# Kernel tuning notes

Measured on AMD Instinct MI355X. Metric: run time of the kernel, lower is better.

Reference implementation:

```python
import jax, jax.numpy as jnp
import numpy as np

N, T, F_IN = 20000, 13, 3
E = 320000
NB, NL = 4, 2
C_RES, C_DIL, C_SKIP, C_END = 32, 32, 256, 512
KSZ, KHOP = 2, 4
N_PRED, N_OUT = 12, 2
L = NB * NL
DILS = [2 ** i for _ in range(NB) for i in range(NL)]  # [1,2,1,2,1,2,1,2]
EPS = 1e-5


def _dconv(x, w, d):
    # x: [N,C,T], w: [O,I,K]; valid dilated conv -> [N,O,T-(K-1)*d]
    return jax.lax.conv_general_dilated(x, w, (1,), 'VALID', rhs_dilation=(d,),
                                        dimension_numbers=('NCH', 'OIH', 'NCH'))


def _forward(inputs, edge_src, edge_dst, enter_w, enter_b, filt_w, filt_b, gate_w, gate_b,
             gc_w, gc_b, skip_w, skip_b, bn_g, bn_b, out1_w, out1_b, out2_w, out2_b):
    # inputs: [N,T,F] -> x: [N,C_RES,T] via 1x1 conv (enter)
    x = jnp.einsum('of,ntf->not', enter_w, inputs) + enter_b[None, :, None]
    deg = jax.ops.segment_sum(jnp.ones((E,), x.dtype), edge_dst, num_segments=N)
    deg = jnp.maximum(deg, 1.0)[:, None, None]

    def propagate(h):  # [N,t,C]: mean over incoming edges (normalized diffusion step)
        return jax.ops.segment_sum(h[edge_src], edge_dst, num_segments=N) / deg

    skip = jnp.zeros((N, C_SKIP, T), x.dtype)
    for l in range(L):
        d = DILS[l]
        f = jnp.tanh(_dconv(x, filt_w[l], d) + filt_b[l][None, :, None])
        g = jax.nn.sigmoid(_dconv(x, gate_w[l], d) + gate_b[l][None, :, None])
        h = f * g                                   # [N,C_DIL,t]
        t = h.shape[-1]
        skip = skip[..., -t:] + jnp.einsum('oc,nct->not', skip_w[l], h) + skip_b[l][None, :, None]
        # K-hop graph diffusion conv on [N,t,C]
        hh = h.transpose(0, 2, 1)
        acc = jnp.einsum('ntc,co->nto', hh, gc_w[l, 0])
        cur = hh
        for k in range(1, KHOP):
            cur = propagate(cur)
            acc = acc + jnp.einsum('ntc,co->nto', cur, gc_w[l, k])
        acc = acc + gc_b[l]
        x = acc.transpose(0, 2, 1) + x[..., -t:]    # residual add
        # BatchNorm1d over (N, t) per channel (training-mode batch stats)
        mu = x.mean(axis=(0, 2), keepdims=True)
        var = x.var(axis=(0, 2), keepdims=True)
        x = bn_g[l][None, :, None] * (x - mu) * jax.lax.rsqrt(var + EPS) + bn_b[l][None, :, None]
    y = jax.nn.relu(skip)                           # [N,C_SKIP,1]
    y = jax.nn.relu(jnp.einsum('oc,nct->not', out1_w, y) + out1_b[None, :, None])
    y = jnp.einsum('oc,nct->not', out2_w, y) + out2_b[None, :, None]  # [N,n_pred*n_out,1]
    return y.reshape(N, N_PRED, -1)


def setup_inputs() -> dict:
    key = jax.random.key(0)
    ks = jax.random.split(key, 12)
    s = 0.05
    f32 = jnp.float32
    return {
        'inputs': jax.random.normal(ks[0], (N, T, F_IN), f32),
        'edge_src': jax.random.randint(ks[1], (E,), 0, N),
        'edge_dst': jax.random.randint(ks[2], (E,), 0, N),
        'enter_w': jax.random.normal(ks[3], (C_RES, F_IN), f32) * s,
        'enter_b': jnp.zeros((C_RES,), f32),
        'filt_w': jax.random.normal(ks[4], (L, C_DIL, C_RES, KSZ), f32) * s,
        'filt_b': jnp.zeros((L, C_DIL), f32),
        'gate_w': jax.random.normal(ks[5], (L, C_DIL, C_RES, KSZ), f32) * s,
        'gate_b': jnp.zeros((L, C_DIL), f32),
        'gc_w': jax.random.normal(ks[6], (L, KHOP, C_DIL, C_RES), f32) * s,
        'gc_b': jnp.zeros((L, C_RES), f32),
        'skip_w': jax.random.normal(ks[7], (L, C_SKIP, C_DIL), f32) * s,
        'skip_b': jnp.zeros((L, C_SKIP), f32),
        'bn_g': jnp.ones((L, C_RES), f32),
        'bn_b': jnp.zeros((L, C_RES), f32),
        'out1_w': jax.random.normal(ks[8], (C_END, C_SKIP), f32) * s,
        'out1_b': jnp.zeros((C_END,), f32),
        'out2_w': jax.random.normal(ks[9], (N_PRED * N_OUT, C_END), f32) * s,
        'out2_b': jnp.zeros((N_PRED * N_OUT,), f32),
    }


def reference(inputs, edge_src, edge_dst, enter_w, enter_b, filt_w, filt_b, gate_w, gate_b,
              gc_w, gc_b, skip_w, skip_b, bn_g, bn_b, out1_w, out1_b, out2_w, out2_b):
    return _forward(inputs, edge_src, edge_dst, enter_w, enter_b, filt_w, filt_b, gate_w, gate_b,
                    gc_w, gc_b, skip_w, skip_b, bn_g, bn_b, out1_w, out1_b, out2_w, out2_b)
```

## Files before the change

### kernel.cpp

```cpp
#include <hip/hip_runtime.h>
#include <cmath>

constexpr int N = 20000, T = 13, E = 320000;
constexpr int NB_SCAN = (N + 255) / 256;
constexpr int NPART = 64;
typedef unsigned int uint32;

typedef __attribute__((ext_vector_type(8))) short short8;
typedef __attribute__((ext_vector_type(4))) float f32x4;

__device__ __forceinline__ unsigned short f2bf(float f) {
  unsigned int u = __float_as_uint(f);
  unsigned int r = (u + 0x7FFFu + ((u >> 16) & 1u)) >> 16;
  return (unsigned short)r;
}
__device__ __forceinline__ float bflo(uint32 v) { return __uint_as_float(v << 16); }
__device__ __forceinline__ float bfhi(uint32 v) { return __uint_as_float(v & 0xFFFF0000u); }
__device__ __forceinline__ uint32 packbf(float lo, float hi) {
  return (uint32)f2bf(lo) | ((uint32)f2bf(hi) << 16);
}

constexpr size_t WALIGN = 512;
constexpr size_t align_up(size_t x) { return (x + WALIGN - 1) & ~(WALIGN - 1); }

constexpr size_t XA_OFF  = 0;
constexpr size_t X_SZ    = align_up((size_t)N * 13 * 32 * 4);
constexpr size_t XB_OFF  = XA_OFF + X_SZ;
constexpr size_t H_OFF   = XB_OFF + X_SZ;
constexpr size_t H_SZ    = align_up((size_t)N * 12 * 32 * 4);
constexpr size_t C1_OFF  = H_OFF + H_SZ;
constexpr size_t C2_OFF  = C1_OFF + H_SZ;
constexpr size_t C3_OFF  = C2_OFF + H_SZ;
constexpr size_t HL_OFF  = C3_OFF + H_SZ;
constexpr size_t HL_SZ   = align_up((size_t)N * 256 * 4);
constexpr size_t WS2_OFF = HL_OFF + HL_SZ;
constexpr size_t SB_OFF  = WS2_OFF + align_up(256 * 256 * 4);
constexpr size_t SUMS_OFF = SB_OFF + align_up(256 * 4);
constexpr size_t PAR_OFF  = SUMS_OFF + align_up(8 * NPART * 64 * 4);
constexpr size_t CNT_OFF  = PAR_OFF + align_up(9 * 64 * 4);
constexpr size_t ROW_OFF  = CNT_OFF + align_up((size_t)N * 4);
constexpr size_t FILL_OFF = ROW_OFF + align_up((size_t)(N + 1) * 4);
constexpr size_t COL_OFF  = FILL_OFF + align_up((size_t)N * 4);
constexpr size_t DEG_OFF  = COL_OFF + align_up((size_t)E * 4);
constexpr size_t BP_OFF   = DEG_OFF + align_up((size_t)N * 4);
constexpr size_t CP_OFF   = BP_OFF + align_up(8 * 2048 * 4);
constexpr size_t BW1_OFF  = CP_OFF + align_up(8 * 2176 * 4);
constexpr size_t BW2_OFF  = BW1_OFF + align_up(32768 * 4);
constexpr size_t BS_OFF   = BW2_OFF + align_up(65536 * 4);
constexpr size_t BO_OFF   = BS_OFF + align_up((size_t)NB_SCAN * 4);
constexpr size_t S_OFF  = C2_OFF;

__global__ void k_count(const int* __restrict__ dst, int* __restrict__ cnt) {
  int i = blockIdx.x * 256 + threadIdx.x;
  if (i < E) atomicAdd(&cnt[dst[i]], 1);
}

__global__ __launch_bounds__(256) void k_scan1(const int* __restrict__ cnt, int* __restrict__ bsum) {
  __shared__ int sc[256];
  int t = threadIdx.x; int idx = blockIdx.x * 256 + t;
  int v = (idx < N) ? cnt[idx] : 0;
  sc[t] = v; __syncthreads();
  for (int off = 1; off < 256; off <<= 1) {
    int u = (t >= off) ? sc[t - off] : 0;
    __syncthreads();
    sc[t] += u;
    __syncthreads();
  }
  if (t == 255) bsum[blockIdx.x] = sc[255];
}

__global__ __launch_bounds__(256) void k_scan2(const int* __restrict__ bsum, int* __restrict__ boff) {
  __shared__ int sc[256];
  int t = threadIdx.x;
  int v = (t < NB_SCAN) ? bsum[t] : 0;
  sc[t] = v; __syncthreads();
  for (int off = 1; off < 256; off <<= 1) {
    int u = (t >= off) ? sc[t - off] : 0;
    __syncthreads();
    sc[t] += u;
    __syncthreads();
  }
  if (t < NB_SCAN) boff[t] = sc[t] - v;
  if (t == 255) boff[NB_SCAN] = sc[255];
}

__global__ __launch_bounds__(256) void k_scan3(const int* __restrict__ cnt, const int* __restrict__ boff,
                                               int* __restrict__ rowptr, int* __restrict__ fill,
                                               float* __restrict__ deginv) {
  __shared__ int sc[256];
  int t = threadIdx.x; int idx = blockIdx.x * 256 + t;
  int v = (idx < N) ? cnt[idx] : 0;
  sc[t] = v; __syncthreads();
  for (int off = 1; off < 256; off <<= 1) {
    int u = (t >= off) ? sc[t - off] : 0;
    __syncthreads();
    sc[t] += u;
    __syncthreads();
  }
  if (idx < N) {
    int run = boff[blockIdx.x] + sc[t] - v;
    rowptr[idx] = run; fill[idx] = run;
    deginv[idx] = 1.0f / (float)(v > 1 ? v : 1);
  }
  if (blockIdx.x == 0 && t == 0) rowptr[N] = boff[NB_SCAN];
}

__global__ void k_scatter(const int* __restrict__ src, const int* __restrict__ dst,
                          int* __restrict__ fill, int* __restrict__ col) {
  int i = blockIdx.x * 256 + threadIdx.x;
  if (i < E) { int d = dst[i]; int p = atomicAdd(&fill[d], 1); col[p] = src[i]; }
}

__global__ void k_init_params(float* __restrict__ par) {
  int i = threadIdx.x;
  par[i] = (i < 32) ? 1.0f : 0.0f;
}

__global__ void k_prep_gcw(const float* __restrict__ gcw, uint32* __restrict__ bp) {
  int idx = blockIdx.x * 256 + threadIdx.x;
  if (idx >= 8 * 4 * 2 * 64 * 4) return;
  int w4 = idx & 3, lane = (idx >> 2) & 63, hh = (idx >> 8) & 1, s = (idx >> 9) & 3, l = idx >> 11;
  int n = lane & 15, q = lane >> 4;
  int k0 = q * 8 + w4 * 2, o = hh * 16 + n;
  const float* g = gcw + (((size_t)(l * 4 + s) * 32 + k0) * 32 + o);
  bp[idx] = packbf(g[0], g[32]);
}

__global__ void k_prep_bw(const float* __restrict__ W, uint32* __restrict__ bp, int O) {
  int idx = blockIdx.x * 256 + threadIdx.x;
  int total = (O / 16) * 8 * 64 * 4;
  if (idx >= total) return;
  int w4 = idx & 3, lane = (idx >> 2) & 63, ks = (idx >> 8) & 7, ot = idx >> 11;
  int n = lane & 15, q = lane >> 4;
  int k = ks * 32 + q * 8 + w4 * 2;
  const float* wr = W + (size_t)(ot * 16 + n) * 256 + k;
  bp[idx] = packbf(wr[0], wr[1]);
}

__global__ void k_prep_w2(const float* __restrict__ W, uint32* __restrict__ bp) {
  int idx = blockIdx.x * 256 + threadIdx.x;
  if (idx >= 2 * 16 * 64 * 4) return;
  int w4 = idx & 3, lane = (idx >> 2) & 63, ks = (idx >> 8) & 15, ot = idx >> 12;
  int n = lane & 15, q = lane >> 4;
  int k = ks * 32 + q * 8 + w4 * 2;
  int o = ot * 16 + n;
  float v0 = 0.0f, v1 = 0.0f;
  if (o < 24) { const float* wr = W + (size_t)o * 512 + k; v0 = wr[0]; v1 = wr[1]; }
  bp[idx] = packbf(v0, v1);
}

__global__ void k_prep_conv(const float* __restrict__ fw, const float* __restrict__ fb,
                            const float* __restrict__ gw, const float* __restrict__ gb,
                            const float* __restrict__ par, int layer, uint32* __restrict__ cpbuf) {
  uint32* base = cpbuf + (size_t)layer * 2176;
  int tid = blockIdx.x * 256 + threadIdx.x;
  if (tid < 2048) {
    int w4 = tid & 3, lane = (tid >> 2) & 63, hh = (tid >> 8) & 1, ktap = (tid >> 9) & 1, sel = tid >> 10;
    int n = lane & 15, q = lane >> 4;
    int c0 = q * 8 + w4 * 2, o = hh * 16 + n;
    const float* w = sel ? gw : fw;
    float sc0 = par[layer * 64 + c0], sc1 = par[layer * 64 + c0 + 1];
    float v0 = w[(((size_t)layer * 32 + o) * 32 + c0) * 2 + ktap] * sc0;
    float v1 = w[(((size_t)layer * 32 + o) * 32 + c0 + 1) * 2 + ktap] * sc1;
    base[tid] = packbf(v0, v1);
  } else if (tid < 2048 + 64) {
    int i = tid - 2048; int sel = i >> 5; int o = i & 31;
    const float* w = sel ? gw : fw;
    const float* b = sel ? gb : fb;
    float s = b[layer * 32 + o];
    for (int c = 0; c < 32; c++) {
      float sh = par[layer * 64 + 32 + c];
      s += (w[(((size_t)layer * 32 + o) * 32 + c) * 2 + 0] +
            w[(((size_t)layer * 32 + o) * 32 + c) * 2 + 1]) * sh;
    }
    ((float*)base)[2048 + i] = s;
  }
}

__global__ void k_enter(const float* __restrict__ in, const float* __restrict__ w,
                        const float* __restrict__ b, uint32* __restrict__ x) {
  int idx = blockIdx.x * 256 + threadIdx.x;
  if (idx >= N * 13 * 16) return;
  int cw = idx & 15; int tmp = idx >> 4; int t = tmp % 13; int n = tmp / 13;
  int c0 = cw * 2;
  const float* ip = in + (size_t)n * (13 * 3) + t * 3;
  float v0 = b[c0]     + w[c0 * 3 + 0]       * ip[0] + w[c0 * 3 + 1]       * ip[1] + w[c0 * 3 + 2]       * ip[2];
  float v1 = b[c0 + 1] + w[(c0 + 1) * 3 + 0] * ip[0] + w[(c0 + 1) * 3 + 1] * ip[1] + w[(c0 + 1) * 3 + 2] * ip[2];
  x[idx] = packbf(v0, v1);
}

template <int TIN, int TOUT, int D>
__global__ __launch_bounds__(256, 4) void k_conv(const uint32* __restrict__ x,
    const uint32* __restrict__ cpbuf, int layer,
    uint32* __restrict__ h, uint32* __restrict__ hlast) {
  constexpr int RS = 34;
  __shared__ float xst[128 * RS];
  int tid = threadIdx.x;
  int wave = tid >> 6, lane = tid & 63;
  int m = lane & 15, q = lane >> 4;
  int nrows = N * TOUT;
  int base = blockIdx.x * 128;

  const uint32* cp = cpbuf + (size_t)layer * 2176;
  short8 bf[2][2][2];
#pragma unroll
  for (int sel = 0; sel < 2; sel++)
#pragma unroll
    for (int kt = 0; kt < 2; kt++)
#pragma unroll
      for (int hh = 0; hh < 2; hh++)
        bf[sel][kt][hh] = *(const short8*)(cp + (size_t)(((sel * 2 + kt) * 2 + hh) * 64 + lane) * 4);
  const float* bias = (const float*)(cp + 2048);
  float fb0 = bias[m], fb1 = bias[16 + m], gb0 = bias[32 + m], gb1 = bias[48 + m];

#pragma unroll
  for (int tile = 0; tile < 2; tile++) {
    int row = base + wave * 32 + tile * 16 + m;
    bool valid = row < nrows;
    int rr = valid ? row : 0;
    int n = rr / TOUT, tt = rr - n * TOUT;
    const uint32* xr = x + ((size_t)n * TIN + tt) * 16 + q * 4;
    short8 a0 = {0,0,0,0,0,0,0,0}, aD = {0,0,0,0,0,0,0,0};
    if (valid) { a0 = *(const short8*)xr; aD = *(const short8*)(xr + D * 16); }
    f32x4 aF0 = {0.f,0.f,0.f,0.f}, aF1 = {0.f,0.f,0.f,0.f};
    f32x4 aG0 = {0.f,0.f,0.f,0.f}, aG1 = {0.f,0.f,0.f,0.f};
    aF0 = __builtin_amdgcn_mfma_f32_16x16x32_bf16(a0, bf[0][0][0], aF0, 0, 0, 0);
    aF0 = __builtin_amdgcn_mfma_f32_16x16x32_bf16(aD, bf[0][1][0], aF0, 0, 0, 0);
    aF1 = __builtin_amdgcn_mfma_f32_16x16x32_bf16(a0, bf[0][0][1], aF1, 0, 0, 0);
    aF1 = __builtin_amdgcn_mfma_f32_16x16x32_bf16(aD, bf[0][1][1], aF1, 0, 0, 0);
    aG0 = __builtin_amdgcn_mfma_f32_16x16x32_bf16(a0, bf[1][0][0], aG0, 0, 0, 0);
    aG0 = __builtin_amdgcn_mfma_f32_16x16x32_bf16(aD, bf[1][1][0], aG0, 0, 0, 0);
    aG1 = __builtin_amdgcn_mfma_f32_16x16x32_bf16(a0, bf[1][0][1], aG1, 0, 0, 0);
    aG1 = __builtin_amdgcn_mfma_f32_16x16x32_bf16(aD, bf[1][1][1], aG1, 0, 0, 0);
#pragma unroll
    for (int r = 0; r < 4; r++) {
      int lrow = wave * 32 + tile * 16 + q * 4 + r;
      float F0 = aF0[r] + fb0, G0 = aG0[r] + gb0;
      float F1 = aF1[r] + fb1, G1 = aG1[r] + gb1;
      float af0 = fabsf(F0), ef0 = __expf(-2.0f * af0);
      float th0 = copysignf((1.0f - ef0) / (1.0f + ef0), F0);
      float hv0 = th0 * (1.0f / (1.0f + __expf(-G0)));
      float af1 = fabsf(F1), ef1 = __expf(-2.0f * af1);
      float th1 = copysignf((1.0f - ef1) / (1.0f + ef1), F1);
      float hv1 = th1 * (1.0f / (1.0f + __expf(-G1)));
      xst[lrow * RS + m]      = hv0;
      xst[lrow * RS + 16 + m] = hv1;
    }
  }
  __syncthreads();
  {
    uint2* outp = (uint2*)h;
#pragma unroll
    for (int it = 0; it < 4; it++) {
      int l = it * 256 + tid;
      int g = base * 8 + l;
      if (g < nrows * 8) {
        int rl = l >> 3, j4 = l & 7;
        float2 a = *(const float2*)&xst[rl * RS + j4 * 4];
        float2 b = *(const float2*)&xst[rl * RS + j4 * 4 + 2];
        uint2 pv = make_uint2(packbf(a.x, a.y), packbf(b.x, b.y));
        outp[g] = pv;
        int grow = base + rl;
        int node = grow / TOUT, tt = grow - node * TOUT;
        if (tt == TOUT - 1) {
          *(uint2*)(hlast + (size_t)node * 128 + layer * 16 + j4 * 2) = pv;
        }
      }
    }
  }
}

template <int F>
__global__ __launch_bounds__(256) void k_hop(const uint32* __restrict__ in, uint32* __restrict__ out,
    const int* __restrict__ rowptr, const int* __restrict__ col, const float* __restrict__ deginv) {
  constexpr int F2 = F / 2;
  constexpr int NW = (F2 + 63) / 64;
  int wid = (blockIdx.x * 256 + threadIdx.x) >> 6;
  int lane = threadIdx.x & 63;
  if (wid >= N) return;
  int s = rowptr[wid], e = rowptr[wid + 1];
  float alo[NW], ahi[NW];
#pragma unroll
  for (int k = 0; k < NW; k++) { alo[k] = 0.0f; ahi[k] = 0.0f; }
  int idx = s;
  for (; idx + 7 < e; idx += 8) {
    const uint32* p[8];
#pragma unroll
    for (int q = 0; q < 8; q++) p[q] = in + (size_t)col[idx + q] * F2;
    uint32 v[8][NW];
#pragma unroll
    for (int q = 0; q < 8; q++) {
#pragma unroll
      for (int k = 0; k < NW; k++) {
        int j = k * 64 + lane;
        v[q][k] = (j < F2) ? p[q][j] : 0u;
      }
    }
#pragma unroll
    for (int k = 0; k < NW; k++) {
      alo[k] += ((bflo(v[0][k]) + bflo(v[1][k])) + (bflo(v[2][k]) + bflo(v[3][k]))) +
                ((bflo(v[4][k]) + bflo(v[5][k])) + (bflo(v[6][k]) + bflo(v[7][k])));
      ahi[k] += ((bfhi(v[0][k]) + bfhi(v[1][k])) + (bfhi(v[2][k]) + bfhi(v[3][k]))) +
                ((bfhi(v[4][k]) + bfhi(v[5][k])) + (bfhi(v[6][k]) + bfhi(v[7][k])));
    }
  }
  for (; idx + 3 < e; idx += 4) {
    const uint32* p0 = in + (size_t)col[idx] * F2;
    const uint32* p1 = in + (size_t)col[idx + 1] * F2;
    const uint32* p2 = in + (size_t)col[idx + 2] * F2;
    const uint32* p3 = in + (size_t)col[idx + 3] * F2;
#pragma unroll
    for (int k = 0; k < NW; k++) {
      int j = k * 64 + lane;
      if (j < F2) {
        uint32 v0 = p0[j], v1 = p1[j], v2 = p2[j], v3 = p3[j];
        alo[k] += (bflo(v0) + bflo(v1)) + (bflo(v2) + bflo(v3));
        ahi[k] += (bfhi(v0) + bfhi(v1)) + (bfhi(v2) + bfhi(v3));
      }
    }
  }
  for (; idx < e; ++idx) {
    const uint32* p = in + (size_t)col[idx] * F2;
#pragma unroll
    for (int k = 0; k < NW; k++) {
      int j = k * 64 + lane;
      if (j < F2) { uint32 v = p[j]; alo[k] += bflo(v); ahi[k] += bfhi(v); }
    }
  }
  float inv = deginv[wid];
  uint32* q = out + (size_t)wid * F2;
#pragma unroll
  for (int k = 0; k < NW; k++) {
    int j = k * 64 + lane;
    if (j < F2) q[j] = packbf(alo[k] * inv, ahi[k] * inv);
  }
}

template <int TIN, int TOUT>
__global__ __launch_bounds__(256, 4) void k_combine(const uint32* __restrict__ h,
    const uint32* __restrict__ c1, const uint32* __restrict__ c2, const uint32* __restrict__ c3,
    const uint32* __restrict__ bpack, const float* __restrict__ gcb,
    const uint32* __restrict__ xcur, int layer,
    const float* __restrict__ par, int slot,
    uint32* __restrict__ xnext, float* __restrict__ sums) {
  constexpr int RS = 34;
  __shared__ float xst[128 * RS];
  __shared__ float pbuf[96];
  __shared__ float r1s[32], r2s[32];
  int tid = threadIdx.x;
  if (tid < 32) {
    pbuf[tid]      = gcb[layer * 32 + tid];
    pbuf[32 + tid] = par[slot * 64 + tid];
    pbuf[64 + tid] = par[slot * 64 + 32 + tid];
    r1s[tid] = 0.0f; r2s[tid] = 0.0f;
  }

  int nrows = N * TOUT;
  int base = blockIdx.x * 128;
  int wave = tid >> 6, lane = tid & 63;
  int m = lane & 15, q = lane >> 4;

  const uint32* bp = bpack + (size_t)layer * 2048;
  short8 bf[4][2];
#pragma unroll
  for (int s = 0; s < 4; s++)
#pragma unroll
    for (int hh = 0; hh < 2; hh++)
      bf[s][hh] = *(const short8*)(bp + (size_t)((s * 2 + hh) * 64 + lane) * 4);

  f32x4 acc[2][2] = {{{0.f,0.f,0.f,0.f},{0.f,0.f,0.f,0.f}},{{0.f,0.f,0.f,0.f},{0.f,0.f,0.f,0.f}}};
  const uint32* srcs[4] = { h, c1, c2, c3 };
#pragma unroll
  for (int s = 0; s < 4; s++) {
    const uint32* sp = srcs[s];
#pragma unroll
    for (int t = 0; t < 2; t++) {
      int row = base + wave * 32 + t * 16 + m;
      short8 af = {0,0,0,0,0,0,0,0};
      if (row < nrows) af = *(const short8*)(sp + (size_t)row * 16 + q * 4);
      acc[t][0] = __builtin_amdgcn_mfma_f32_16x16x32_bf16(af, bf[s][0], acc[t][0], 0, 0, 0);
      acc[t][1] = __builtin_amdgcn_mfma_f32_16x16x32_bf16(af, bf[s][1], acc[t][1], 0, 0, 0);
    }
  }

  __syncthreads();
#pragma unroll
  for (int t = 0; t < 2; t++)
#pragma unroll
    for (int hh = 0; hh < 2; hh++)
#pragma unroll
      for (int r = 0; r < 4; r++)
        xst[(wave * 32 + t * 16 + q * 4 + r) * RS + hh * 16 + m] = acc[t][hh][r];
  __syncthreads();

  constexpr int toff = TIN - TOUT;
  int rg = tid >> 3, oq = tid & 7;
  float gb0 = pbuf[oq * 4 + 0], gb1 = pbuf[oq * 4 + 1], gb2 = pbuf[oq * 4 + 2], gb3 = pbuf[oq * 4 + 3];
  float sc0 = pbuf[32 + oq * 4 + 0], sc1 = pbuf[32 + oq * 4 + 1], sc2 = pbuf[32 + oq * 4 + 2], sc3 = pbuf[32 + oq * 4 + 3];
  float sh0 = pbuf[64 + oq * 4 + 0], sh1 = pbuf[64 + oq * 4 + 1], sh2 = pbuf[64 + oq * 4 + 2], sh3 = pbuf[64 + oq * 4 + 3];
  float s1[4] = {0.f, 0.f, 0.f, 0.f}, s2[4] = {0.f, 0.f, 0.f, 0.f};
#pragma unroll
  for (int i = 0; i < 4; i++) {
    int r = rg + 32 * i;
    int row = base + r;
    bool act = row < nrows;
    float2 aa = *(const float2*)&xst[r * RS + oq * 4];
    float2 ab = *(const float2*)&xst[r * RS + oq * 4 + 2];
    float xr0 = 0.f, xr1 = 0.f, xr2 = 0.f, xr3 = 0.f;
    if (act) {
      int node = row / TOUT, t_ = row - node * TOUT;
      const uint32* rp = xcur + ((size_t)node * TIN + toff + t_) * 16 + oq * 2;
      uint32 va = rp[0], vb = rp[1];
      xr0 = bflo(va); xr1 = bfhi(va); xr2 = bflo(vb); xr3 = bfhi(vb);
    }
    float v0 = aa.x + gb0 + sc0 * xr0 + sh0;
    float v1 = aa.y + gb1 + sc1 * xr1 + sh1;
    float v2 = ab.x + gb2 + sc2 * xr2 + sh2;
    float v3 = ab.y + gb3 + sc3 * xr3 + sh3;
    *(float2*)&xst[r * RS + oq * 4]     = make_float2(v0, v1);
    *(float2*)&xst[r * RS + oq * 4 + 2] = make_float2(v2, v3);
    if (act) {
      s1[0] += v0; s1[1] += v1; s1[2] += v2; s1[3] += v3;
      s2[0] += v0 * v0; s2[1] += v1 * v1; s2[2] += v2 * v2; s2[3] += v3 * v3;
    }
  }
#pragma unroll
  for (int j = 0; j < 4; j++) {
    atomicAdd(&r1s[oq * 4 + j], s1[j]);
    atomicAdd(&r2s[oq * 4 + j], s2[j]);
  }
  __syncthreads();

  {
    uint2* outp = (uint2*)xnext;
#pragma unroll
    for (int it = 0; it < 4; it++) {
      int l = it * 256 + tid;
      int g = base * 8 + l;
      if (g < nrows * 8) {
        int rl = l >> 3, j4 = l & 7;
        float2 a = *(const float2*)&xst[rl * RS + j4 * 4];
        float2 b = *(const float2*)&xst[rl * RS + j4 * 4 + 2];
        outp[g] = make_uint2(packbf(a.x, a.y), packbf(b.x, b.y));
      }
    }
  }
  {
    int part = blockIdx.x & (NPART - 1);
    float* sp = sums + ((size_t)layer * NPART + part) * 64;
    if (tid < 32) atomicAdd(&sp[tid], r1s[tid]);
    else if (tid < 64) atomicAdd(&sp[tid], r2s[tid - 32]);
  }
}

__global__ void k_bnfin(const float* __restrict__ sums, const float* __restrict__ bng,
                        const float* __restrict__ bnb, float* __restrict__ par,
                        int layer, int tout) {
  int o = threadIdx.x;
  float cnt = (float)N * (float)tout;
  float s1 = 0.0f, s2 = 0.0f;
  const float* lp = sums + (size_t)layer * NPART * 64;
  for (int p = 0; p < NPART; p++) {
    s1 += lp[p * 64 + o];
    s2 += lp[p * 64 + 32 + o];
  }
  float mu = s1 / cnt;
  float var = s2 / cnt - mu * mu;
  float sc = bng[layer * 32 + o] * rsqrtf(var + 1e-5f);
  par[(layer + 1) * 64 + o] = sc;
  par[(layer + 1) * 64 + 32 + o] = bnb[layer * 32 + o] - mu * sc;
}

__global__ void k_prep_skipw(const float* __restrict__ sw, float* __restrict__ w2) {
  int idx = blockIdx.x * 256 + threadIdx.x;
  if (idx >= 8 * 256 * 32) return;
  int l = idx / (256 * 32), r = idx % (256 * 32), o = r / 32, c = r & 31;
  w2[o * 256 + l * 32 + c] = sw[idx];
}
__global__ void k_prep_sb(const float* __restrict__ sb, float* __restrict__ out) {
  int o = threadIdx.x;
  float s = 0.0f;
  for (int l = 0; l < 8; l++) s += sb[l * 256 + o];
  out[o] = s;
}

__global__ __launch_bounds__(256) void k_gemm1(const uint32* __restrict__ A,
    const uint32* __restrict__ bp, const float* __restrict__ bias, uint32* __restrict__ Sb) {
  constexpr int RS = 68;
  __shared__ float xst[128 * RS];
  int tid = threadIdx.x;
  int wave = tid >> 6, lane = tid & 63;
  int m = lane & 15, q = lane >> 4;
  int base = blockIdx.x * 128;
  int ot0 = blockIdx.y * 8;

  f32x4 acc[2][8];
#pragma unroll
  for (int t = 0; t < 2; t++)
#pragma unroll
    for (int nt = 0; nt < 8; nt++) acc[t][nt] = (f32x4){0.f, 0.f, 0.f, 0.f};

  int row0 = base + wave * 32 + m;
  int row1 = row0 + 16;
#pragma unroll 1
  for (int ks = 0; ks < 8; ks++) {
    short8 a0 = {0,0,0,0,0,0,0,0}, a1 = {0,0,0,0,0,0,0,0};
    if (row0 < N) a0 = *(const short8*)(A + (size_t)row0 * 128 + ks * 16 + q * 4);
    if (row1 < N) a1 = *(const short8*)(A + (size_t)row1 * 128 + ks * 16 + q * 4);
#pragma unroll
    for (int nt = 0; nt < 8; nt++) {
      short8 b = *(const short8*)(bp + (size_t)(((ot0 + nt) * 8 + ks) * 64 + lane) * 4);
      acc[0][nt] = __builtin_amdgcn_mfma_f32_16x16x32_bf16(a0, b, acc[0][nt], 0, 0, 0);
      acc[1][nt] = __builtin_amdgcn_mfma_f32_16x16x32_bf16(a1, b, acc[1][nt], 0, 0, 0);
    }
  }

#pragma unroll
  for (int half = 0; half < 2; half++) {
    if (half) __syncthreads();
#pragma unroll
    for (int t = 0; t < 2; t++)
#pragma unroll
      for (int nn = 0; nn < 4; nn++) {
        float bv = bias[blockIdx.y * 128 + (half * 4 + nn) * 16 + m];
#pragma unroll
        for (int r = 0; r < 4; r++) {
          float v = acc[t][half * 4 + nn][r] + bv;
          xst[(wave * 32 + t * 16 + q * 4 + r) * RS + nn * 16 + m] = fmaxf(v, 0.0f);
        }
      }
    __syncthreads();
#pragma unroll
    for (int it = 0; it < 8; it++) {
      int l = it * 256 + tid;
      int rl = l >> 4, c4 = l & 15;
      int grow = base + rl;
      if (grow < N) {
        float2 a = *(const float2*)&xst[rl * RS + c4 * 4];
        float2 b = *(const float2*)&xst[rl * RS + c4 * 4 + 2];
        *(uint2*)(Sb + (size_t)grow * 128 + blockIdx.y * 64 + half * 32 + c4 * 2) =
            make_uint2(packbf(a.x, a.y), packbf(b.x, b.y));
      }
    }
  }
}

__global__ __launch_bounds__(256) void k_gemm2f(const uint32* __restrict__ A,
    const uint32* __restrict__ bp, const float* __restrict__ bias,
    const uint32* __restrict__ w2p, const float* __restrict__ b2, float* __restrict__ out) {
  constexpr int RS = 68;
  __shared__ float xst[128 * RS];
  int tid = threadIdx.x;
  int wave = tid >> 6, lane = tid & 63;
  int m = lane & 15, q = lane >> 4;
  int base = blockIdx.x * 128;
  int ot0 = blockIdx.y * 8;

  f32x4 acc[2][8];
#pragma unroll
  for (int t = 0; t < 2; t++)
#pragma unroll
    for (int nt = 0; nt < 8; nt++) acc[t][nt] = (f32x4){0.f, 0.f, 0.f, 0.f};

  int row0 = base + wave * 32 + m;
  int row1 = row0 + 16;
#pragma unroll 1
  for (int ks = 0; ks < 8; ks++) {
    short8 a0 = {0,0,0,0,0,0,0,0}, a1 = {0,0,0,0,0,0,0,0};
    if (row0 < N) a0 = *(const short8*)(A + (size_t)row0 * 128 + ks * 16 + q * 4);
    if (row1 < N) a1 = *(const short8*)(A + (size_t)row1 * 128 + ks * 16 + q * 4);
#pragma unroll
    for (int nt = 0; nt < 8; nt++) {
      short8 b = *(const short8*)(bp + (size_t)(((ot0 + nt) * 8 + ks) * 64 + lane) * 4);
      acc[0][nt] = __builtin_amdgcn_mfma_f32_16x16x32_bf16(a0, b, acc[0][nt], 0, 0, 0);
      acc[1][nt] = __builtin_amdgcn_mfma_f32_16x16x32_bf16(a1, b, acc[1][nt], 0, 0, 0);
    }
  }

  f32x4 acc2[2][2];
#pragma unroll
  for (int t = 0; t < 2; t++)
#pragma unroll
    for (int o2 = 0; o2 < 2; o2++) acc2[t][o2] = (f32x4){0.f, 0.f, 0.f, 0.f};

#pragma unroll
  for (int half = 0; half < 2; half++) {
    if (half) __syncthreads();
#pragma unroll
    for (int t = 0; t < 2; t++)
#pragma unroll
      for (int nn = 0; nn < 4; nn++) {
        float bv = bias[blockIdx.y * 128 + (half * 4 + nn) * 16 + m];
#pragma unroll
        for (int r = 0; r < 4; r++) {
          float v = acc[t][half * 4 + nn][r] + bv;
          xst[(wave * 32 + t * 16 + q * 4 + r) * RS + nn * 16 + m] = fmaxf(v, 0.0f);
        }
      }
    __syncthreads();
#pragma unroll
    for (int kl = 0; kl < 2; kl++) {
      short8 a2[2];
#pragma unroll
      for (int t = 0; t < 2; t++) {
        const float* xp = &xst[(size_t)(wave * 32 + t * 16 + m) * RS + kl * 32 + q * 8];
        float4 f0 = *(const float4*)xp;
        float4 f1 = *(const float4*)(xp + 4);
        uint32 u[4];
        u[0] = packbf(f0.x, f0.y); u[1] = packbf(f0.z, f0.w);
        u[2] = packbf(f1.x, f1.y); u[3] = packbf(f1.z, f1.w);
        a2[t] = *(const short8*)u;
      }
      int ksg = blockIdx.y * 4 + half * 2 + kl;
#pragma unroll
      for (int o2 = 0; o2 < 2; o2++) {
        short8 b = *(const short8*)(w2p + (size_t)(((o2 * 16 + ksg) * 64 + lane) * 4));
        acc2[0][o2] = __builtin_amdgcn_mfma_f32_16x16x32_bf16(a2[0], b, acc2[0][o2], 0, 0, 0);
        acc2[1][o2] = __builtin_amdgcn_mfma_f32_16x16x32_bf16(a2[1], b, acc2[1][o2], 0, 0, 0);
      }
    }
  }

#pragma unroll
  for (int t = 0; t < 2; t++)
#pragma unroll
    for (int o2 = 0; o2 < 2; o2++) {
      int oc = o2 * 16 + m;
      if (oc < 24) {
#pragma unroll
        for (int r = 0; r < 4; r++) {
          int row = base + wave * 32 + t * 16 + q * 4 + r;
          if (row < N) {
            float v = acc2[t][o2][r];
            if (blockIdx.y == 0) v += b2[oc];
            atomicAdd(&out[(size_t)row * 24 + oc], v);
          }
        }
      }
    }
}

struct Ptrs {
  const float *fw, *fb, *gw, *gb, *gcb, *bng, *bnb;
  const uint32 *bpack;
  uint32 *cpack;
  void *H, *C1, *C2, *C3;
  uint32 *HL;
  float *par, *sums;
  const int *row, *col;
  const float *deg;
};

template <int TIN, int TOUT, int D>
static void run_layer(int layer, bool last, const Ptrs& P, uint32*& xc, uint32*& xn, hipStream_t stream) {
  int cblocks = (N * TOUT + 127) / 128;
  k_conv<TIN, TOUT, D><<<cblocks, 256, 0, stream>>>(xc, P.cpack, layer, (uint32*)P.H, P.HL);
  if (!last) {
    constexpr int F = TOUT * 32;
    int hb = (N * 64 + 255) / 256;
    k_hop<F><<<hb, 256, 0, stream>>>((const uint32*)P.H, (uint32*)P.C1, P.row, P.col, P.deg);
    k_hop<F><<<hb, 256, 0, stream>>>((const uint32*)P.C1, (uint32*)P.C2, P.row, P.col, P.deg);
    k_hop<F><<<hb, 256, 0, stream>>>((const uint32*)P.C2, (uint32*)P.C3, P.row, P.col, P.deg);
    k_combine<TIN, TOUT><<<cblocks, 256, 0, stream>>>((const uint32*)P.H, (const uint32*)P.C1,
                                                      (const uint32*)P.C2, (const uint32*)P.C3,
                                                      P.bpack, P.gcb, xc, layer, P.par, layer, xn, P.sums);
    k_bnfin<<<1, 32, 0, stream>>>(P.sums, P.bng, P.bnb, P.par, layer, TOUT);
    k_prep_conv<<<9, 256, 0, stream>>>(P.fw, P.fb, P.gw, P.gb, P.par, layer + 1, P.cpack);
    uint32* tmp = xc; xc = xn; xn = tmp;
  }
}

extern "C" void kernel_launch(void* const* d_in, const int* in_sizes, int n_in,
                              void* d_out, int out_size, void* d_ws, size_t ws_size,
                              hipStream_t stream) {
  const float* inputs  = (const float*)d_in[0];
  const int*   esrc    = (const int*)d_in[1];
  const int*   edst    = (const int*)d_in[2];
  const float* enter_w = (const float*)d_in[3];
  const float* enter_b = (const float*)d_in[4];
  const float* filt_w  = (const float*)d_in[5];
  const float* filt_b  = (const float*)d_in[6];
  const float* gate_w  = (const float*)d_in[7];
  const float* gate_b  = (const float*)d_in[8];
  const float* gc_w    = (const float*)d_in[9];
  const float* gc_b    = (const float*)d_in[10];
  const float* skip_w  = (const float*)d_in[11];
  const float* skip_b  = (const float*)d_in[12];
  const float* bn_g    = (const float*)d_in[13];
  const float* bn_b    = (const float*)d_in[14];
  const float* out1_w  = (const float*)d_in[15];
  const float* out1_b  = (const float*)d_in[16];
  const float* out2_w  = (const float*)d_in[17];
  const float* out2_b  = (const float*)d_in[18];

  char* ws = (char*)d_ws;
  uint32* XA = (uint32*)(ws + XA_OFF);
  uint32* XB = (uint32*)(ws + XB_OFF);
  void* H    = (void*)(ws + H_OFF);
  void* C1   = (void*)(ws + C1_OFF);
  void* C2   = (void*)(ws + C2_OFF);
  void* C3   = (void*)(ws + C3_OFF);
  uint32* HLB = (uint32*)(ws + HL_OFF);
  float* WS2 = (float*)(ws + WS2_OFF);
  float* SB  = (float*)(ws + SB_OFF);
  float* SUMS = (float*)(ws + SUMS_OFF);
  float* PAR  = (float*)(ws + PAR_OFF);
  int* CNT  = (int*)(ws + CNT_OFF);
  int* ROW  = (int*)(ws + ROW_OFF);
  int* FILL = (int*)(ws + FILL_OFF);
  int* COL  = (int*)(ws + COL_OFF);
  float* DEG = (float*)(ws + DEG_OFF);
  uint32* BP = (uint32*)(ws + BP_OFF);
  uint32* CP = (uint32*)(ws + CP_OFF);
  uint32* BW1 = (uint32*)(ws + BW1_OFF);
  uint32* BW2 = (uint32*)(ws + BW2_OFF);
  int* BS = (int*)(ws + BS_OFF);
  int* BO = (int*)(ws + BO_OFF);
  uint32* Sb  = (uint32*)(ws + S_OFF);
  uint32* W2P = (uint32*)(ws + WS2_OFF);

  hipMemsetAsync(CNT, 0, (size_t)N * 4, stream);
  hipMemsetAsync(SUMS, 0, (size_t)8 * NPART * 64 * 4, stream);
  hipMemsetAsync(d_out, 0, (size_t)out_size * 4, stream);

  k_count<<<(E + 255) / 256, 256, 0, stream>>>(edst, CNT);
  k_scan1<<<NB_SCAN, 256, 0, stream>>>(CNT, BS);
  k_scan2<<<1, 256, 0, stream>>>(BS, BO);
  k_scan3<<<NB_SCAN, 256, 0, stream>>>(CNT, BO, ROW, FILL, DEG);
  k_scatter<<<(E + 255) / 256, 256, 0, stream>>>(esrc, edst, FILL, COL);
  k_init_params<<<1, 64, 0, stream>>>(PAR);
  k_prep_gcw<<<(8 * 4 * 2 * 64 * 4 + 255) / 256, 256, 0, stream>>>(gc_w, BP);
  k_prep_conv<<<9, 256, 0, stream>>>(filt_w, filt_b, gate_w, gate_b, PAR, 0, CP);
  k_enter<<<(N * 13 * 16 + 255) / 256, 256, 0, stream>>>(inputs, enter_w, enter_b, XA);
  k_prep_skipw<<<(8 * 256 * 32 + 255) / 256, 256, 0, stream>>>(skip_w, WS2);
  k_prep_sb<<<1, 256, 0, stream>>>(skip_b, SB);
  k_prep_bw<<<(32768 + 255) / 256, 256, 0, stream>>>(WS2, BW1, 256);
  k_prep_bw<<<(65536 + 255) / 256, 256, 0, stream>>>(out1_w, BW2, 512);
  k_prep_w2<<<(8192 + 255) / 256, 256, 0, stream>>>(out2_w, W2P);

  Ptrs P;
  P.fw = filt_w; P.fb = filt_b; P.gw = gate_w; P.gb = gate_b;
  P.gcb = gc_b; P.bng = bn_g; P.bnb = bn_b; P.bpack = BP; P.cpack = CP;
  P.H = H; P.C1 = C1; P.C2 = C2; P.C3 = C3; P.HL = HLB; P.par = PAR; P.sums = SUMS;
  P.row = ROW; P.col = COL; P.deg = DEG;

  uint32* xc = XA; uint32* xn = XB;
  run_layer<13, 12, 1>(0, false, P, xc, xn, stream);
  run_layer<12, 10, 2>(1, false, P, xc, xn, stream);
  run_layer<10, 9, 1>(2, false, P, xc, xn, stream);
  run_layer<9, 7, 2>(3, false, P, xc, xn, stream);
  run_layer<7, 6, 1>(4, false, P, xc, xn, stream);
  run_layer<6, 4, 2>(5, false, P, xc, xn, stream);
  run_layer<4, 3, 1>(6, false, P, xc, xn, stream);
  run_layer<3, 1, 2>(7, true, P, xc, xn, stream);

  dim3 g1((N + 127) / 128, 2);
  k_gemm1<<<g1, 256, 0, stream>>>(HLB, BW1, SB, Sb);
  dim3 g2((N + 127) / 128, 4);
  k_gemm2f<<<g2, 256, 0, stream>>>(Sb, BW2, out1_b, W2P, out2_b, (float*)d_out);
}
```

Before: 974.0 us.

## Merge setup kernels and fold BN finalize into last combine block

Replaces three memsets and about ten small prep/enter kernels with a single block-partitioned k_setup kernel. It merges scan2 into scan3 by having each block redo the short block-sum scan. It also drops the per-layer k_bnfin and k_prep_conv launches by having the last-finishing k_combine block, found through an atomic done counter, compute the BN scale and shift and repack the next layer's conv weights. The goal is to cut launch count and serialized tiny kernels, at the cost of a last-block reduction tail and extra memory fences.

Result: slower. 1.591 ms (+63.3%).

```diff
diff --git a/kernel.cpp b/kernel.cpp
--- a/kernel.cpp
+++ b/kernel.cpp
@@ -33,8 +33,8 @@
 constexpr size_t C3_OFF  = C2_OFF + H_SZ;
 constexpr size_t HL_OFF  = C3_OFF + H_SZ;
 constexpr size_t HL_SZ   = align_up((size_t)N * 256 * 4);
-constexpr size_t WS2_OFF = HL_OFF + HL_SZ;
-constexpr size_t SB_OFF  = WS2_OFF + align_up(256 * 256 * 4);
+constexpr size_t W2P_OFF = HL_OFF + HL_SZ;
+constexpr size_t SB_OFF  = W2P_OFF + align_up(8192 * 4);
 constexpr size_t SUMS_OFF = SB_OFF + align_up(256 * 4);
 constexpr size_t PAR_OFF  = SUMS_OFF + align_up(8 * NPART * 64 * 4);
 constexpr size_t CNT_OFF  = PAR_OFF + align_up(9 * 64 * 4);
@@ -47,8 +47,103 @@
 constexpr size_t BW1_OFF  = CP_OFF + align_up(8 * 2176 * 4);
 constexpr size_t BW2_OFF  = BW1_OFF + align_up(32768 * 4);
 constexpr size_t BS_OFF   = BW2_OFF + align_up(65536 * 4);
-constexpr size_t BO_OFF   = BS_OFF + align_up((size_t)NB_SCAN * 4);
+constexpr size_t DONE_OFF = BS_OFF + align_up((size_t)NB_SCAN * 4);
 constexpr size_t S_OFF  = C2_OFF;
+
+constexpr int SU_CNT1 = 20;
+constexpr int SU_SUM1 = SU_CNT1 + 33;
+constexpr int SU_OUT1 = SU_SUM1 + 469;
+constexpr int SU_PAR1 = SU_OUT1 + 1;
+constexpr int SU_GCW1 = SU_PAR1 + 64;
+constexpr int SU_BW11 = SU_GCW1 + 128;
+constexpr int SU_BW21 = SU_BW11 + 256;
+constexpr int SU_W21  = SU_BW21 + 32;
+constexpr int SU_SB1  = SU_W21 + 1;
+constexpr int SU_CV1  = SU_SB1 + 9;
+constexpr int SU_EN1  = SU_CV1 + 16250;
+
+__global__ __launch_bounds__(256) void k_setup(
+    const float* __restrict__ inputs, const float* __restrict__ enter_w, const float* __restrict__ enter_b,
+    const float* __restrict__ filt_w, const float* __restrict__ filt_b,
+    const float* __restrict__ gate_w, const float* __restrict__ gate_b,
+    const float* __restrict__ gc_w, const float* __restrict__ skip_w, const float* __restrict__ skip_b,
+    const float* __restrict__ out1_w, const float* __restrict__ out2_w,
+    int* __restrict__ cnt, float* __restrict__ sums, int* __restrict__ done,
+    float* __restrict__ dout, int out_sz,
+    float* __restrict__ par, uint32* __restrict__ bp, uint32* __restrict__ bw1,
+    uint32* __restrict__ bw2, uint32* __restrict__ w2p, float* __restrict__ sbias,
+    uint32* __restrict__ cpack, uint32* __restrict__ x) {
+  int b = blockIdx.x, tid = threadIdx.x;
+  if (b < SU_CNT1) {
+    int i = b * 256 + tid;
+    if (i < 5000) ((int4*)cnt)[i] = make_int4(0, 0, 0, 0);
+  } else if (b < SU_SUM1) {
+    int i = (b - SU_CNT1) * 256 + tid;
+    if (i < 8192) ((float4*)sums)[i] = make_float4(0.f, 0.f, 0.f, 0.f);
+    else if (i < 8200) done[i - 8192] = 0;
+  } else if (b < SU_OUT1) {
+    int i = (b - SU_SUM1) * 256 + tid;
+    if (i < (out_sz >> 2)) ((float4*)dout)[i] = make_float4(0.f, 0.f, 0.f, 0.f);
+  } else if (b < SU_PAR1) {
+    if (tid < 64) par[tid] = (tid < 32) ? 1.0f : 0.0f;
+  } else if (b < SU_GCW1) {
+    int idx = (b - SU_PAR1) * 256 + tid;
+    int w4 = idx & 3, lane = (idx >> 2) & 63, hh = (idx >> 8) & 1, s = (idx >> 9) & 3, l = idx >> 11;
+    int n = lane & 15, q = lane >> 4;
+    int k0 = q * 8 + w4 * 2, o = hh * 16 + n;
+    const float* g = gc_w + (((size_t)(l * 4 + s) * 32 + k0) * 32 + o);
+    bp[idx] = packbf(g[0], g[32]);
+  } else if (b < SU_BW11) {
+    int idx = (b - SU_GCW1) * 256 + tid;
+    int w4 = idx & 3, lane = (idx >> 2) & 63, ks = (idx >> 8) & 7, ot = idx >> 11;
+    int n = lane & 15, q = lane >> 4;
+    int c = q * 8 + w4 * 2, o = ot * 16 + n;
+    const float* wr = skip_w + ((size_t)ks * 256 + o) * 32 + c;
+    bw1[idx] = packbf(wr[0], wr[1]);
+  } else if (b < SU_BW21) {
+    int idx = (b - SU_BW11) * 256 + tid;
+    int w4 = idx & 3, lane = (idx >> 2) & 63, ks = (idx >> 8) & 7, ot = idx >> 11;
+    int n = lane & 15, q = lane >> 4;
+    int k = ks * 32 + q * 8 + w4 * 2;
+    const float* wr = out1_w + (size_t)(ot * 16 + n) * 256 + k;
+    bw2[idx] = packbf(wr[0], wr[1]);
+  } else if (b < SU_W21) {
+    int idx = (b - SU_BW21) * 256 + tid;
+    int w4 = idx & 3, lane = (idx >> 2) & 63, ks = (idx >> 8) & 15, ot = idx >> 12;
+    int n = lane & 15, q = lane >> 4;
+    int k = ks * 32 + q * 8 + w4 * 2;
+    int o = ot * 16 + n;
+    float v0 = 0.0f, v1 = 0.0f;
+    if (o < 24) { const float* wr = out2_w + (size_t)o * 512 + k; v0 = wr[0]; v1 = wr[1]; }
+    w2p[idx] = packbf(v0, v1);
+  } else if (b < SU_SB1) {
+    float s = 0.0f;
+    for (int l = 0; l < 8; l++) s += skip_b[l * 256 + tid];
+    sbias[tid] = s;
+  } else if (b < SU_CV1) {
+    int i = (b - SU_SB1) * 256 + tid;
+    if (i < 2048) {
+      int w4 = i & 3, lane = (i >> 2) & 63, hh = (i >> 8) & 1, ktap = (i >> 9) & 1, sel = i >> 10;
+      int n = lane & 15, q = lane >> 4;
+      int c0 = q * 8 + w4 * 2, o = hh * 16 + n;
+      const float* w = sel ? gate_w : filt_w;
+      float v0 = w[((size_t)o * 32 + c0) * 2 + ktap];
+      float v1 = w[((size_t)o * 32 + c0 + 1) * 2 + ktap];
+      cpack[i] = packbf(v0, v1);
+    } else if (i < 2112) {
+      int j = i - 2048; int sel = j >> 5; int o = j & 31;
+      ((float*)cpack)[2048 + j] = sel ? gate_b[o] : filt_b[o];
+    }
+  } else {
+    int idx = (b - SU_CV1) * 256 + tid;
+    int cw = idx & 15; int tmp = idx >> 4; int t = tmp % 13; int n = tmp / 13;
+    int c0 = cw * 2;
+    const float* ip = inputs + (size_t)n * (13 * 3) + t * 3;
+    float v0 = enter_b[c0]     + enter_w[c0 * 3 + 0]       * ip[0] + enter_w[c0 * 3 + 1]       * ip[1] + enter_w[c0 * 3 + 2]       * ip[2];
+    float v1 = enter_b[c0 + 1] + enter_w[(c0 + 1) * 3 + 0] * ip[0] + enter_w[(c0 + 1) * 3 + 1] * ip[1] + enter_w[(c0 + 1) * 3 + 2] * ip[2];
+    x[idx] = packbf(v0, v1);
+  }
+}
 
 __global__ void k_count(const int* __restrict__ dst, int* __restrict__ cnt) {
   int i = blockIdx.x * 256 + threadIdx.x;
@@ -69,124 +164,42 @@
   if (t == 255) bsum[blockIdx.x] = sc[255];
 }
 
-__global__ __launch_bounds__(256) void k_scan2(const int* __restrict__ bsum, int* __restrict__ boff) {
-  __shared__ int sc[256];
-  int t = threadIdx.x;
-  int v = (t < NB_SCAN) ? bsum[t] : 0;
-  sc[t] = v; __syncthreads();
-  for (int off = 1; off < 256; off <<= 1) {
-    int u = (t >= off) ? sc[t - off] : 0;
-    __syncthreads();
-    sc[t] += u;
-    __syncthreads();
-  }
-  if (t < NB_SCAN) boff[t] = sc[t] - v;
-  if (t == 255) boff[NB_SCAN] = sc[255];
-}
-
-__global__ __launch_bounds__(256) void k_scan3(const int* __restrict__ cnt, const int* __restrict__ boff,
+__global__ __launch_bounds__(256) void k_scan3(const int* __restrict__ cnt, const int* __restrict__ bsum,
                                                int* __restrict__ rowptr, int* __restrict__ fill,
                                                float* __restrict__ deginv) {
   __shared__ int sc[256];
+  __shared__ int bo[128];
   int t = threadIdx.x; int idx = blockIdx.x * 256 + t;
+  if (t < 128) bo[t] = (t < NB_SCAN) ? bsum[t] : 0;
   int v = (idx < N) ? cnt[idx] : 0;
   sc[t] = v; __syncthreads();
-  for (int off = 1; off < 256; off <<= 1) {
-    int u = (t >= off) ? sc[t - off] : 0;
+  for (int off = 1; off < 128; off <<= 1) {
+    int u1 = (t < 128 && t >= off) ? bo[t - off] : 0;
+    int u2 = (t >= off) ? sc[t - off] : 0;
     __syncthreads();
-    sc[t] += u;
+    if (t < 128) bo[t] += u1;
+    sc[t] += u2;
     __syncthreads();
   }
+  {
+    int u2 = (t >= 128) ? sc[t - 128] : 0;
+    __syncthreads();
+    sc[t] += u2;
+    __syncthreads();
+  }
   if (idx < N) {
-    int run = boff[blockIdx.x] + sc[t] - v;
+    int myoff = bo[blockIdx.x] - bsum[blockIdx.x];
+    int run = myoff + sc[t] - v;
     rowptr[idx] = run; fill[idx] = run;
     deginv[idx] = 1.0f / (float)(v > 1 ? v : 1);
   }
-  if (blockIdx.x == 0 && t == 0) rowptr[N] = boff[NB_SCAN];
+  if (blockIdx.x == 0 && t == 0) rowptr[N] = bo[NB_SCAN - 1];
 }
 
 __global__ void k_scatter(const int* __restrict__ src, const int* __restrict__ dst,
                           int* __restrict__ fill, int* __restrict__ col) {
   int i = blockIdx.x * 256 + threadIdx.x;
   if (i < E) { int d = dst[i]; int p = atomicAdd(&fill[d], 1); col[p] = src[i]; }
-}
-
-__global__ void k_init_params(float* __restrict__ par) {
-  int i = threadIdx.x;
-  par[i] = (i < 32) ? 1.0f : 0.0f;
-}
-
-__global__ void k_prep_gcw(const float* __restrict__ gcw, uint32* __restrict__ bp) {
-  int idx = blockIdx.x * 256 + threadIdx.x;
-  if (idx >= 8 * 4 * 2 * 64 * 4) return;
-  int w4 = idx & 3, lane = (idx >> 2) & 63, hh = (idx >> 8) & 1, s = (idx >> 9) & 3, l = idx >> 11;
-  int n = lane & 15, q = lane >> 4;
-  int k0 = q * 8 + w4 * 2, o = hh * 16 + n;
-  const float* g = gcw + (((size_t)(l * 4 + s) * 32 + k0) * 32 + o);
-  bp[idx] = packbf(g[0], g[32]);
-}
-
-__global__ void k_prep_bw(const float* __restrict__ W, uint32* __restrict__ bp, int O) {
-  int idx = blockIdx.x * 256 + threadIdx.x;
-  int total = (O / 16) * 8 * 64 * 4;
-  if (idx >= total) return;
-  int w4 = idx & 3, lane = (idx >> 2) & 63, ks = (idx >> 8) & 7, ot = idx >> 11;
-  int n = lane & 15, q = lane >> 4;
-  int k = ks * 32 + q * 8 + w4 * 2;
-  const float* wr = W + (size_t)(ot * 16 + n) * 256 + k;
-  bp[idx] = packbf(wr[0], wr[1]);
-}
-
-__global__ void k_prep_w2(const float* __restrict__ W, uint32* __restrict__ bp) {
-  int idx = blockIdx.x * 256 + threadIdx.x;
-  if (idx >= 2 * 16 * 64 * 4) return;
-  int w4 = idx & 3, lane = (idx >> 2) & 63, ks = (idx >> 8) & 15, ot = idx >> 12;
-  int n = lane & 15, q = lane >> 4;
-  int k = ks * 32 + q * 8 + w4 * 2;
-  int o = ot * 16 + n;
-  float v0 = 0.0f, v1 = 0.0f;
-  if (o < 24) { const float* wr = W + (size_t)o * 512 + k; v0 = wr[0]; v1 = wr[1]; }
-  bp[idx] = packbf(v0, v1);
-}
-
-__global__ void k_prep_conv(const float* __restrict__ fw, const float* __restrict__ fb,
-                            const float* __restrict__ gw, const float* __restrict__ gb,
-                            const float* __restrict__ par, int layer, uint32* __restrict__ cpbuf) {
-  uint32* base = cpbuf + (size_t)layer * 2176;
-  int tid = blockIdx.x * 256 + threadIdx.x;
-  if (tid < 2048) {
-    int w4 = tid & 3, lane = (tid >> 2) & 63, hh = (tid >> 8) & 1, ktap = (tid >> 9) & 1, sel = tid >> 10;
-    int n = lane & 15, q = lane >> 4;
-    int c0 = q * 8 + w4 * 2, o = hh * 16 + n;
-    const float* w = sel ? gw : fw;
-    float sc0 = par[layer * 64 + c0], sc1 = par[layer * 64 + c0 + 1];
-    float v0 = w[(((size_t)layer * 32 + o) * 32 + c0) * 2 + ktap] * sc0;
-    float v1 = w[(((size_t)layer * 32 + o) * 32 + c0 + 1) * 2 + ktap] * sc1;
-    base[tid] = packbf(v0, v1);
-  } else if (tid < 2048 + 64) {
-    int i = tid - 2048; int sel = i >> 5; int o = i & 31;
-    const float* w = sel ? gw : fw;
-    const float* b = sel ? gb : fb;
-    float s = b[layer * 32 + o];
-    for (int c = 0; c < 32; c++) {
-      float sh = par[layer * 64 + 32 + c];
-      s += (w[(((size_t)layer * 32 + o) * 32 + c) * 2 + 0] +
-            w[(((size_t)layer * 32 + o) * 32 + c) * 2 + 1]) * sh;
-    }
-    ((float*)base)[2048 + i] = s;
-  }
-}
-
-__global__ void k_enter(const float* __restrict__ in, const float* __restrict__ w,
-                        const float* __restrict__ b, uint32* __restrict__ x) {
-  int idx = blockIdx.x * 256 + threadIdx.x;
-  if (idx >= N * 13 * 16) return;
-  int cw = idx & 15; int tmp = idx >> 4; int t = tmp % 13; int n = tmp / 13;
-  int c0 = cw * 2;
-  const float* ip = in + (size_t)n * (13 * 3) + t * 3;
-  float v0 = b[c0]     + w[c0 * 3 + 0]       * ip[0] + w[c0 * 3 + 1]       * ip[1] + w[c0 * 3 + 2]       * ip[2];
-  float v1 = b[c0 + 1] + w[(c0 + 1) * 3 + 0] * ip[0] + w[(c0 + 1) * 3 + 1] * ip[1] + w[(c0 + 1) * 3 + 2] * ip[2];
-  x[idx] = packbf(v0, v1);
 }
 
 template <int TIN, int TOUT, int D>
@@ -341,17 +354,22 @@
     const uint32* __restrict__ c1, const uint32* __restrict__ c2, const uint32* __restrict__ c3,
     const uint32* __restrict__ bpack, const float* __restrict__ gcb,
     const uint32* __restrict__ xcur, int layer,
-    const float* __restrict__ par, int slot,
-    uint32* __restrict__ xnext, float* __restrict__ sums) {
+    float* __restrict__ par,
+    uint32* __restrict__ xnext, float* __restrict__ sums, int* __restrict__ done,
+    const float* __restrict__ bng, const float* __restrict__ bnb,
+    const float* __restrict__ fw, const float* __restrict__ fb,
+    const float* __restrict__ gw, const float* __restrict__ gb,
+    uint32* __restrict__ cpack) {
   constexpr int RS = 34;
   __shared__ float xst[128 * RS];
   __shared__ float pbuf[96];
   __shared__ float r1s[32], r2s[32];
+  __shared__ int lastflag;
   int tid = threadIdx.x;
   if (tid < 32) {
     pbuf[tid]      = gcb[layer * 32 + tid];
-    pbuf[32 + tid] = par[slot * 64 + tid];
-    pbuf[64 + tid] = par[slot * 64 + 32 + tid];
+    pbuf[32 + tid] = par[layer * 64 + tid];
+    pbuf[64 + tid] = par[layer * 64 + 32 + tid];
     r1s[tid] = 0.0f; r2s[tid] = 0.0f;
   }
 
@@ -451,37 +469,70 @@
     if (tid < 32) atomicAdd(&sp[tid], r1s[tid]);
     else if (tid < 64) atomicAdd(&sp[tid], r2s[tid - 32]);
   }
-}
-
-__global__ void k_bnfin(const float* __restrict__ sums, const float* __restrict__ bng,
-                        const float* __restrict__ bnb, float* __restrict__ par,
-                        int layer, int tout) {
-  int o = threadIdx.x;
-  float cnt = (float)N * (float)tout;
-  float s1 = 0.0f, s2 = 0.0f;
-  const float* lp = sums + (size_t)layer * NPART * 64;
-  for (int p = 0; p < NPART; p++) {
-    s1 += lp[p * 64 + o];
-    s2 += lp[p * 64 + 32 + o];
-  }
-  float mu = s1 / cnt;
-  float var = s2 / cnt - mu * mu;
-  float sc = bng[layer * 32 + o] * rsqrtf(var + 1e-5f);
-  par[(layer + 1) * 64 + o] = sc;
-  par[(layer + 1) * 64 + 32 + o] = bnb[layer * 32 + o] - mu * sc;
-}
-
-__global__ void k_prep_skipw(const float* __restrict__ sw, float* __restrict__ w2) {
-  int idx = blockIdx.x * 256 + threadIdx.x;
-  if (idx >= 8 * 256 * 32) return;
-  int l = idx / (256 * 32), r = idx % (256 * 32), o = r / 32, c = r & 31;
-  w2[o * 256 + l * 32 + c] = sw[idx];
-}
-__global__ void k_prep_sb(const float* __restrict__ sb, float* __restrict__ out) {
-  int o = threadIdx.x;
-  float s = 0.0f;
-  for (int l = 0; l < 8; l++) s += sb[l * 256 + o];
-  out[o] = s;
+
+  __threadfence();
+  if (tid == 0) {
+    int c = atomicAdd(&done[layer], 1);
+    lastflag = (c == (int)gridDim.x - 1) ? 1 : 0;
+  }
+  __syncthreads();
+  if (!lastflag) return;
+  __threadfence();
+
+  __shared__ float red1[8][32];
+  __shared__ float red2[8][32];
+  {
+    int o = tid & 31, grp = tid >> 5;
+    float t1 = 0.f, t2 = 0.f;
+    float* lp = sums + (size_t)layer * NPART * 64;
+    for (int p = grp; p < NPART; p += 8) {
+      t1 += atomicAdd(&lp[p * 64 + o], 0.0f);
+      t2 += atomicAdd(&lp[p * 64 + 32 + o], 0.0f);
+    }
+    red1[grp][o] = t1; red2[grp][o] = t2;
+  }
+  __syncthreads();
+  __shared__ float pb[64];
+  if (tid < 32) {
+    float t1 = 0.f, t2 = 0.f;
+#pragma unroll
+    for (int g = 0; g < 8; g++) { t1 += red1[g][tid]; t2 += red2[g][tid]; }
+    float cnt = (float)N * (float)TOUT;
+    float mu = t1 / cnt;
+    float var = t2 / cnt - mu * mu;
+    float sc = bng[layer * 32 + tid] * rsqrtf(var + 1e-5f);
+    float sh = bnb[layer * 32 + tid] - mu * sc;
+    par[(layer + 1) * 64 + tid] = sc;
+    par[(layer + 1) * 64 + 32 + tid] = sh;
+    pb[tid] = sc; pb[32 + tid] = sh;
+  }
+  __syncthreads();
+  {
+    int nl = layer + 1;
+    uint32* cbase = cpack + (size_t)nl * 2176;
+    for (int tix = tid; tix < 2048 + 64; tix += 256) {
+      if (tix < 2048) {
+        int w4 = tix & 3, lane2 = (tix >> 2) & 63, hh2 = (tix >> 8) & 1, ktap = (tix >> 9) & 1, sel = tix >> 10;
+        int n2 = lane2 & 15, q2 = lane2 >> 4;
+        int c0 = q2 * 8 + w4 * 2, o = hh2 * 16 + n2;
+        const float* w = sel ? gw : fw;
+        float v0 = w[(((size_t)nl * 32 + o) * 32 + c0) * 2 + ktap] * pb[c0];
+        float v1 = w[(((size_t)nl * 32 + o) * 32 + c0 + 1) * 2 + ktap] * pb[c0 + 1];
+        cbase[tix] = packbf(v0, v1);
+      } else {
+        int i = tix - 2048; int sel = i >> 5; int o = i & 31;
+        const float* w = sel ? gw : fw;
+        const float* b = sel ? gb : fb;
+        float s = b[nl * 32 + o];
+        for (int c = 0; c < 32; c++) {
+          float sh2 = pb[32 + c];
+          s += (w[(((size_t)nl * 32 + o) * 32 + c) * 2 + 0] +
+                w[(((size_t)nl * 32 + o) * 32 + c) * 2 + 1]) * sh2;
+        }
+        ((float*)cbase)[2048 + i] = s;
+      }
+    }
+  }
 }
 
 __global__ __launch_bounds__(256) void k_gemm1(const uint32* __restrict__ A,
@@ -647,6 +698,7 @@
   void *H, *C1, *C2, *C3;
   uint32 *HL;
   float *par, *sums;
+  int *done;
   const int *row, *col;
   const float *deg;
 };
@@ -663,9 +715,9 @@
     k_hop<F><<<hb, 256, 0, stream>>>((const uint32*)P.C2, (uint32*)P.C3, P.row, P.col, P.deg);
     k_combine<TIN, TOUT><<<cblocks, 256, 0, stream>>>((const uint32*)P.H, (const uint32*)P.C1,
                                                       (const uint32*)P.C2, (const uint32*)P.C3,
-                                                      P.bpack, P.gcb, xc, layer, P.par, layer, xn, P.sums);
-    k_bnfin<<<1, 32, 0, stream>>>(P.sums, P.bng, P.bnb, P.par, layer, TOUT);
-    k_prep_conv<<<9, 256, 0, stream>>>(P.fw, P.fb, P.gw, P.gb, P.par, layer + 1, P.cpack);
+                                                      P.bpack, P.gcb, xc, layer, P.par, xn, P.sums,
+                                                      P.done, P.bng, P.bnb, P.fw, P.fb, P.gw, P.gb,
+                                                      P.cpack);
     uint32* tmp = xc; xc = xn; xn = tmp;
   }
 }
@@ -701,7 +753,7 @@
   void* C2   = (void*)(ws + C2_OFF);
   void* C3   = (void*)(ws + C3_OFF);
   uint32* HLB = (uint32*)(ws + HL_OFF);
-  float* WS2 = (float*)(ws + WS2_OFF);
+  uint32* W2P = (uint32*)(ws + W2P_OFF);
   float* SB  = (float*)(ws + SB_OFF);
   float* SUMS = (float*)(ws + SUMS_OFF);
   float* PAR  = (float*)(ws + PAR_OFF);
@@ -715,34 +767,24 @@
   uint32* BW1 = (uint32*)(ws + BW1_OFF);
   uint32* BW2 = (uint32*)(ws + BW2_OFF);
   int* BS = (int*)(ws + BS_OFF);
-  int* BO = (int*)(ws + BO_OFF);
+  int* DONE = (int*)(ws + DONE_OFF);
   uint32* Sb  = (uint32*)(ws + S_OFF);
-  uint32* W2P = (uint32*)(ws + WS2_OFF);
-
-  hipMemsetAsync(CNT, 0, (size_t)N * 4, stream);
-  hipMemsetAsync(SUMS, 0, (size_t)8 * NPART * 64 * 4, stream);
-  hipMemsetAsync(d_out, 0, (size_t)out_size * 4, stream);
+
+  k_setup<<<SU_EN1, 256, 0, stream>>>(inputs, enter_w, enter_b, filt_w, filt_b, gate_w, gate_b,
+                                      gc_w, skip_w, skip_b, out1_w, out2_w,
+                                      CNT, SUMS, DONE, (float*)d_out, out_size,
+                                      PAR, BP, BW1, BW2, W2P, SB, CP, XA);
 
   k_count<<<(E + 255) / 256, 256, 0, stream>>>(edst, CNT);
   k_scan1<<<NB_SCAN, 256, 0, stream>>>(CNT, BS);
-  k_scan2<<<1, 256, 0, stream>>>(BS, BO);
-  k_scan3<<<NB_SCAN, 256, 0, stream>>>(CNT, BO, ROW, FILL, DEG);
+  k_scan3<<<NB_SCAN, 256, 0, stream>>>(CNT, BS, ROW, FILL, DEG);
   k_scatter<<<(E + 255) / 256, 256, 0, stream>>>(esrc, edst, FILL, COL);
-  k_init_params<<<1, 64, 0, stream>>>(PAR);
-  k_prep_gcw<<<(8 * 4 * 2 * 64 * 4 + 255) / 256, 256, 0, stream>>>(gc_w, BP);
-  k_prep_conv<<<9, 256, 0, stream>>>(filt_w, filt_b, gate_w, gate_b, PAR, 0, CP);
-  k_enter<<<(N * 13 * 16 + 255) / 256, 256, 0, stream>>>(inputs, enter_w, enter_b, XA);
-  k_prep_skipw<<<(8 * 256 * 32 + 255) / 256, 256, 0, stream>>>(skip_w, WS2);
-  k_prep_sb<<<1, 256, 0, stream>>>(skip_b, SB);
-  k_prep_bw<<<(32768 + 255) / 256, 256, 0, stream>>>(WS2, BW1, 256);
-  k_prep_bw<<<(65536 + 255) / 256, 256, 0, stream>>>(out1_w, BW2, 512);
-  k_prep_w2<<<(8192 + 255) / 256, 256, 0, stream>>>(out2_w, W2P);
 
   Ptrs P;
   P.fw = filt_w; P.fb = filt_b; P.gw = gate_w; P.gb = gate_b;
   P.gcb = gc_b; P.bng = bn_g; P.bnb = bn_b; P.bpack = BP; P.cpack = CP;
   P.H = H; P.C1 = C1; P.C2 = C2; P.C3 = C3; P.HL = HLB; P.par = PAR; P.sums = SUMS;
-  P.row = ROW; P.col = COL; P.deg = DEG;
+  P.done = DONE; P.row = ROW; P.col = COL; P.deg = DEG;
 
   uint32* xc = XA; uint32* xn = XB;
   run_layer<13, 12, 1>(0, false, P, xc, xn, stream);
```
